# Kernel optimization log

Measured on AMD Instinct MI355X. Metric: run time of the kernel, lower is better.

The kernel has to match this reference:

```python
import jax, jax.numpy as jnp
import numpy as np

BN_EPS = 1e-5
NN_EPS = 1e-8
K = 3


def conv_bn_relu(x, W, b, gamma, beta, mean, var):
    # x: [B, Cin, N]; W: [Cout, Cin] (1x1 conv); BN in inference mode w/ running stats
    y = jnp.einsum('bcn,oc->bon', x, W) + b[None, :, None]
    y = (y - mean[None, :, None]) * (gamma / jnp.sqrt(var + BN_EPS))[None, :, None] + beta[None, :, None]
    return jax.nn.relu(y)


def three_interpolation(p1, p2, f2):
    # p1: [B, N1, 3] unknown xyz; p2: [B, N2, 3] known xyz; f2: [B, C, N2]
    # squared pairwise distances via the expansion trick (avoids [B,N1,N2,3])
    d2 = (jnp.sum(p1 * p1, -1)[:, :, None]
          + jnp.sum(p2 * p2, -1)[:, None, :]
          - 2.0 * jnp.einsum('bnd,bmd->bnm', p1, p2))  # [B, N1, N2]
    neg_d2, idx = jax.lax.top_k(-d2, K)                 # 3 nearest
    dist = -neg_d2                                      # squared dists, [B, N1, 3]
    recip = 1.0 / (dist + NN_EPS)
    weight = recip / jnp.sum(recip, axis=-1, keepdims=True)  # [B, N1, 3]
    f2t = jnp.transpose(f2, (0, 2, 1))                  # [B, N2, C]
    gathered = jax.vmap(lambda f, i: f[i])(f2t, idx)    # [B, N1, 3, C]
    return jnp.einsum('bnkc,bnk->bcn', gathered, weight)  # [B, C, N1]


def setup_inputs() -> dict:
    key = jax.random.key(0)
    ks = jax.random.split(key, 16)
    B, N1, N2 = 8, 16384, 4096
    mlp = [256, 128, 128]
    inp = {
        'p1': jax.random.normal(ks[0], (B, N1, 3), jnp.float32),
        'p2': jax.random.normal(ks[1], (B, N2, 3), jnp.float32),
        'f2': jax.random.normal(ks[2], (B, mlp[0], N2), jnp.float32),
    }
    kidx = 3
    for li in range(len(mlp) - 1):
        cin, cout = mlp[li], mlp[li + 1]
        inp[f'W{li}'] = jax.random.normal(ks[kidx], (cout, cin), jnp.float32) * (1.0 / np.sqrt(cin)); kidx += 1
        inp[f'b{li}'] = jnp.zeros((cout,), jnp.float32)
        inp[f'gamma{li}'] = jnp.ones((cout,), jnp.float32)
        inp[f'beta{li}'] = jnp.zeros((cout,), jnp.float32)
        inp[f'mean{li}'] = jax.random.normal(ks[kidx], (cout,), jnp.float32) * 0.1; kidx += 1
        inp[f'var{li}'] = jax.random.uniform(ks[kidx], (cout,), jnp.float32, 0.5, 1.5); kidx += 1
    return inp


def reference(p1, p2, f2,
              W0, b0, gamma0, beta0, mean0, var0,
              W1, b1, gamma1, beta1, mean1, var1):
    f = conv_bn_relu(f2, W0, b0, gamma0, beta0, mean0, var0)
    f = conv_bn_relu(f, W1, b1, gamma1, beta1, mean1, var1)
    return three_interpolation(p1, p2, f)
```

## Files before the change

kernel.cpp:

```cpp
#include <hip/hip_runtime.h>

#define B_    8
#define N1_   16384
#define N2_   4096
#define NTOT_ (B_ * N1_)

__device__ __forceinline__ float np_sumsq(float x, float y, float z)
{
#pragma clang fp contract(off)
    return ((x * x + y * y) + z * z);
}

__global__ __launch_bounds__(256) void prep_kernel(
    const float* __restrict__ W0, const float* __restrict__ b0,
    const float* __restrict__ g0, const float* __restrict__ be0,
    const float* __restrict__ m0, const float* __restrict__ v0,
    const float* __restrict__ W1, const float* __restrict__ b1,
    const float* __restrict__ g1, const float* __restrict__ be1,
    const float* __restrict__ m1, const float* __restrict__ v1,
    const float* __restrict__ p2,
    float* __restrict__ W0p, float* __restrict__ b0p,
    float* __restrict__ W1p, float* __restrict__ b1p,
    float4* __restrict__ q4)
{
    const int bx = blockIdx.x;
    const int tid = threadIdx.x;
    if (bx < 128) {
        const int t = bx * 256 + tid;
        const int o = t >> 8;
        const float s = g0[o] / sqrtf(v0[o] + 1e-5f);
        W0p[t] = W0[t] * s;
        if (t < 128) {
            const float ss = g0[t] / sqrtf(v0[t] + 1e-5f);
            b0p[t] = be0[t] + (b0[t] - m0[t]) * ss;
        }
    } else if (bx < 192) {
        const int t = (bx - 128) * 256 + tid;
        const int o = t >> 7;
        const float s = g1[o] / sqrtf(v1[o] + 1e-5f);
        W1p[t] = W1[t] * s;
        if (t < 128) {
            const float ss = g1[t] / sqrtf(v1[t] + 1e-5f);
            b1p[t] = be1[t] + (b1[t] - m1[t]) * ss;
        }
    } else {
        const int t = (bx - 192) * 256 + tid;
        const float x = p2[3 * (size_t)t + 0];
        const float y = p2[3 * (size_t)t + 1];
        const float z = p2[3 * (size_t)t + 2];
        q4[t] = make_float4(x, y, z, np_sumsq(x, y, z));
    }
}

template <int CIN, bool TRANS>
__global__ __launch_bounds__(256) void gemm_relu_kernel(
    const float* __restrict__ X, const float* __restrict__ Wp,
    const float* __restrict__ bp, float* __restrict__ Y)
{
    __shared__ float A_lds[32][136];
    __shared__ float B_lds[32][64];

    const int b  = blockIdx.y;
    const int n0 = blockIdx.x * 64;
    const int tid = threadIdx.x;
    const int ty = tid >> 4;
    const int tx = tid & 15;
    const float* Xb = X + (size_t)b * CIN * N2_;

    float acc[8][4];
#pragma unroll
    for (int i = 0; i < 8; ++i)
#pragma unroll
        for (int j = 0; j < 4; ++j) acc[i][j] = 0.f;

    const int a_kq = (tid & 7) * 4;
    const int a_r0 = tid >> 3;
    const int b_n4 = (tid & 15) * 4;
    const int b_k0 = tid >> 4;

    for (int k0 = 0; k0 < CIN; k0 += 32) {
#pragma unroll
        for (int i = 0; i < 4; ++i) {
            const int row = a_r0 + 32 * i;
            const float4 v = *(const float4*)&Wp[(size_t)row * CIN + k0 + a_kq];
            A_lds[a_kq + 0][row] = v.x;
            A_lds[a_kq + 1][row] = v.y;
            A_lds[a_kq + 2][row] = v.z;
            A_lds[a_kq + 3][row] = v.w;
        }
#pragma unroll
        for (int i = 0; i < 2; ++i) {
            const int krow = b_k0 + 16 * i;
            *(float4*)&B_lds[krow][b_n4] =
                *(const float4*)&Xb[(size_t)(k0 + krow) * N2_ + n0 + b_n4];
        }
        __syncthreads();

#pragma unroll
        for (int kk = 0; kk < 32; ++kk) {
            const float4 a0 = *(const float4*)&A_lds[kk][ty * 4];
            const float4 a1 = *(const float4*)&A_lds[kk][64 + ty * 4];
            const float4 bq = *(const float4*)&B_lds[kk][tx * 4];
            const float av[8] = {a0.x, a0.y, a0.z, a0.w, a1.x, a1.y, a1.z, a1.w};
            const float bv[4] = {bq.x, bq.y, bq.z, bq.w};
#pragma unroll
            for (int i = 0; i < 8; ++i)
#pragma unroll
                for (int j = 0; j < 4; ++j)
                    acc[i][j] = fmaf(av[i], bv[j], acc[i][j]);
        }
        __syncthreads();
    }

    float bias_v[8];
#pragma unroll
    for (int i = 0; i < 8; ++i) {
        const int r = (i < 4) ? (ty * 4 + i) : (64 + ty * 4 + (i - 4));
        bias_v[i] = bp[r];
    }

    if (!TRANS) {
#pragma unroll
        for (int i = 0; i < 8; ++i) {
            const int r = (i < 4) ? (ty * 4 + i) : (64 + ty * 4 + (i - 4));
            float* yrow = Y + ((size_t)b * 128 + r) * N2_ + n0;
            float4 v0;
            v0.x = fmaxf(acc[i][0] + bias_v[i], 0.f);
            v0.y = fmaxf(acc[i][1] + bias_v[i], 0.f);
            v0.z = fmaxf(acc[i][2] + bias_v[i], 0.f);
            v0.w = fmaxf(acc[i][3] + bias_v[i], 0.f);
            *(float4*)(yrow + tx * 4) = v0;
        }
    } else {
        float (*T)[132] = (float(*)[132])&A_lds[0][0];
#pragma unroll
        for (int s = 0; s < 2; ++s) {
            if ((tx >> 3) == s) {
                const int cl0 = (tx & 7) * 4;
#pragma unroll
                for (int i = 0; i < 8; ++i) {
                    const int r = (i < 4) ? (ty * 4 + i) : (64 + ty * 4 + (i - 4));
#pragma unroll
                    for (int j = 0; j < 4; ++j)
                        T[cl0 + j][r] = fmaxf(acc[i][j] + bias_v[i], 0.f);
                }
            }
            __syncthreads();
#pragma unroll
            for (int p = 0; p < 4; ++p) {
                const int row = (tid >> 5) + 8 * p;
                const float4 v = *(const float4*)&T[row][(tid & 31) * 4];
                float* orow = Y + ((size_t)b * N2_ + n0 + 32 * s + row) * 128;
                *(float4*)&orow[(tid & 31) * 4] = v;
            }
            __syncthreads();
        }
    }
}

__global__ __launch_bounds__(256, 8) void knn_phase1(
    const float* __restrict__ p1, const float4* __restrict__ q4,
    float* __restrict__ part_d, int* __restrict__ part_i)
{
    __shared__ float4 qs[1024];
    const int tid = threadIdx.x;
    const int chunk = blockIdx.x & 3;
    const int g = (blockIdx.x >> 2) * 256 + tid;
    const int b = g >> 14;

    const float px = p1[3 * (size_t)g + 0];
    const float py = p1[3 * (size_t)g + 1];
    const float pz = p1[3 * (size_t)g + 2];
    const float s1 = np_sumsq(px, py, pz);

    const float4* qb = q4 + (size_t)b * N2_ + chunk * 1024;
#pragma unroll
    for (int i = 0; i < 4; ++i) qs[tid + i * 256] = qb[tid + i * 256];
    __syncthreads();

    float d0 = 1e30f, d1 = 1e30f, d2v = 1e30f;
    int i0 = 0, i1 = 0, i2 = 0;
    const int jbase = chunk * 1024;

    for (int j = 0; j < 1024; j += 4) {
#pragma unroll
        for (int u = 0; u < 4; ++u) {
            const float4 q = qs[j + u];
            const float dot = __fmaf_rn(px, q.x, __fmaf_rn(py, q.y, __fmul_rn(pz, q.z)));
            const float ss  = s1 + q.w;
            const float t   = __fmaf_rn(-2.0f, dot, ss);
            if (t < d2v) {
                const int jj = jbase + j + u;
                const bool c1 = t < d1, c0 = t < d0;
                d2v = c1 ? d1 : t;                 i2 = c1 ? i1 : jj;
                const float nd1 = c1 ? (c0 ? d0 : t) : d1;
                const int   ni1 = c1 ? (c0 ? i0 : jj) : i1;
                d1 = nd1;                          i1 = ni1;
                d0 = c0 ? t : d0;                  i0 = c0 ? jj : i0;
            }
        }
    }

    part_d[(0 * 4 + chunk) * NTOT_ + g] = d0;
    part_d[(1 * 4 + chunk) * NTOT_ + g] = d1;
    part_d[(2 * 4 + chunk) * NTOT_ + g] = d2v;
    part_i[(0 * 4 + chunk) * NTOT_ + g] = i0;
    part_i[(1 * 4 + chunk) * NTOT_ + g] = i1;
    part_i[(2 * 4 + chunk) * NTOT_ + g] = i2;
}

__global__ __launch_bounds__(256) void gather_kernel(
    const float* __restrict__ f_t, const float* __restrict__ part_d,
    const int* __restrict__ part_i, float* __restrict__ out)
{
    const int tid = threadIdx.x;
    const int lane = tid & 63, cg = tid >> 6;
    const int vb = (blockIdx.x & 7) * 256 + (blockIdx.x >> 3);
    const int g = vb * 64 + lane;
    const int b = g >> 14, n = g & 16383;

    float d0 = 1e30f, d1 = 1e30f, d2v = 1e30f;
    int i0 = 0, i1 = 0, i2 = 0;
#pragma unroll
    for (int c = 0; c < 4; ++c) {
#pragma unroll
        for (int k = 0; k < 3; ++k) {
            const float t = part_d[(k * 4 + c) * NTOT_ + g];
            const int  jj = part_i[(k * 4 + c) * NTOT_ + g];
            if (t < d2v) {
                const bool c1 = t < d1, c0 = t < d0;
                d2v = c1 ? d1 : t;                 i2 = c1 ? i1 : jj;
                const float nd1 = c1 ? (c0 ? d0 : t) : d1;
                const int   ni1 = c1 ? (c0 ? i0 : jj) : i1;
                d1 = nd1;                          i1 = ni1;
                d0 = c0 ? t : d0;                  i0 = c0 ? jj : i0;
            }
        }
    }

    float w0, w1, w2;
    {
#pragma clang fp contract(off)
        const float r0 = 1.0f / (d0 + 1e-8f);
        const float r1 = 1.0f / (d1 + 1e-8f);
        const float r2 = 1.0f / (d2v + 1e-8f);
        const float rs = (r0 + r1) + r2;
        w0 = r0 / rs;
        w1 = r1 / rs;
        w2 = r2 / rs;
    }

    const float* base = f_t + (size_t)b * N2_ * 128 + cg * 32;
    const float4* r0v = (const float4*)(base + (size_t)i0 * 128);
    const float4* r1v = (const float4*)(base + (size_t)i1 * 128);
    const float4* r2v = (const float4*)(base + (size_t)i2 * 128);

    float acc[32];
#pragma unroll
    for (int q = 0; q < 8; ++q) {
        const float4 a = r0v[q], bb = r1v[q], c = r2v[q];
        acc[4 * q + 0] = fmaf(w0, a.x, fmaf(w1, bb.x, w2 * c.x));
        acc[4 * q + 1] = fmaf(w0, a.y, fmaf(w1, bb.y, w2 * c.y));
        acc[4 * q + 2] = fmaf(w0, a.z, fmaf(w1, bb.z, w2 * c.z));
        acc[4 * q + 3] = fmaf(w0, a.w, fmaf(w1, bb.w, w2 * c.w));
    }

    float* ob = out + ((size_t)b * 128 + cg * 32) * N1_ + n;
#pragma unroll
    for (int c = 0; c < 32; ++c)
        __builtin_nontemporal_store(acc[c], ob + (size_t)c * N1_);
}

extern "C" void kernel_launch(void* const* d_in, const int* in_sizes, int n_in,
                              void* d_out, int out_size, void* d_ws, size_t ws_size,
                              hipStream_t stream)
{
    const float* p1  = (const float*)d_in[0];
    const float* p2  = (const float*)d_in[1];
    const float* f2  = (const float*)d_in[2];
    const float* W0  = (const float*)d_in[3];
    const float* b0  = (const float*)d_in[4];
    const float* g0  = (const float*)d_in[5];
    const float* be0 = (const float*)d_in[6];
    const float* m0  = (const float*)d_in[7];
    const float* v0  = (const float*)d_in[8];
    const float* W1  = (const float*)d_in[9];
    const float* b1  = (const float*)d_in[10];
    const float* g1  = (const float*)d_in[11];
    const float* be1 = (const float*)d_in[12];
    const float* m1  = (const float*)d_in[13];
    const float* v1  = (const float*)d_in[14];

    char* ws = (char*)d_ws;
    float4* q4  = (float4*)(ws);
    float*  W0p = (float*)(ws + (512 << 10));
    float*  b0p = (float*)(ws + (640 << 10));
    float*  W1p = (float*)(ws + (644 << 10));
    float*  b1p = (float*)(ws + (708 << 10));
    float*  h   = (float*)(ws + ((size_t)1 << 20));
    float*  f_t = (float*)(ws + ((size_t)17 << 20));
    float*  pd  = (float*)(ws + ((size_t)1 << 20));
    int*    pi  = (int*)  (ws + ((size_t)9 << 20));

    prep_kernel<<<320, 256, 0, stream>>>(W0, b0, g0, be0, m0, v0,
                                         W1, b1, g1, be1, m1, v1,
                                         p2, W0p, b0p, W1p, b1p, q4);

    gemm_relu_kernel<256, false><<<dim3(64, 8), 256, 0, stream>>>(f2, W0p, b0p, h);
    gemm_relu_kernel<128, true ><<<dim3(64, 8), 256, 0, stream>>>(h, W1p, b1p, f_t);

    knn_phase1<<<(NTOT_ / 256) * 4, 256, 0, stream>>>(p1, q4, pd, pi);
    gather_kernel<<<NTOT_ / 64, 256, 0, stream>>>(f_t, pd, pi, (float*)d_out);
}
```

Before: 354.4 us.

## Co-schedule KNN distance chunks with the two 1x1-conv GEMMs in mixed kernels

Merges each GEMM+ReLU stage with half of the KNN phase-1 work into a single launch. Blocks below 512 run the GEMM and the remaining blocks scan two of the four point chunks, sharing a union of LDS buffers. The aim is to fill the GPU, since each GEMM alone launches only 512 blocks, and to drop one kernel launch. The partial-result buffers move to new workspace offsets so they no longer alias h. A __launch_bounds__ occupancy hint of 6 is added, which may constrain registers for the KNN path.

```diff
diff --git a/kernel.cpp b/kernel.cpp
--- a/kernel.cpp
+++ b/kernel.cpp
@@ -52,161 +52,166 @@
     }
 }
 
-template <int CIN, bool TRANS>
-__global__ __launch_bounds__(256) void gemm_relu_kernel(
+template <int PHASE>
+__global__ __launch_bounds__(256, 6) void mix_kernel(
     const float* __restrict__ X, const float* __restrict__ Wp,
-    const float* __restrict__ bp, float* __restrict__ Y)
-{
-    __shared__ float A_lds[32][136];
-    __shared__ float B_lds[32][64];
-
-    const int b  = blockIdx.y;
-    const int n0 = blockIdx.x * 64;
+    const float* __restrict__ bp, float* __restrict__ Y,
+    const float* __restrict__ p1, const float4* __restrict__ q4,
+    float* __restrict__ part_d, int* __restrict__ part_i)
+{
+    constexpr int  CIN   = (PHASE == 1) ? 256 : 128;
+    constexpr bool TRANS = (PHASE == 2);
+
+    __shared__ union LdsU {
+        struct { float A[32][136]; float B[32][64]; } g;
+        float4 qs[1024];
+    } lds;
+
     const int tid = threadIdx.x;
-    const int ty = tid >> 4;
-    const int tx = tid & 15;
-    const float* Xb = X + (size_t)b * CIN * N2_;
-
-    float acc[8][4];
-#pragma unroll
-    for (int i = 0; i < 8; ++i)
-#pragma unroll
-        for (int j = 0; j < 4; ++j) acc[i][j] = 0.f;
-
-    const int a_kq = (tid & 7) * 4;
-    const int a_r0 = tid >> 3;
-    const int b_n4 = (tid & 15) * 4;
-    const int b_k0 = tid >> 4;
-
-    for (int k0 = 0; k0 < CIN; k0 += 32) {
-#pragma unroll
-        for (int i = 0; i < 4; ++i) {
-            const int row = a_r0 + 32 * i;
-            const float4 v = *(const float4*)&Wp[(size_t)row * CIN + k0 + a_kq];
-            A_lds[a_kq + 0][row] = v.x;
-            A_lds[a_kq + 1][row] = v.y;
-            A_lds[a_kq + 2][row] = v.z;
-            A_lds[a_kq + 3][row] = v.w;
-        }
-#pragma unroll
-        for (int i = 0; i < 2; ++i) {
-            const int krow = b_k0 + 16 * i;
-            *(float4*)&B_lds[krow][b_n4] =
-                *(const float4*)&Xb[(size_t)(k0 + krow) * N2_ + n0 + b_n4];
-        }
-        __syncthreads();
-
-#pragma unroll
-        for (int kk = 0; kk < 32; ++kk) {
-            const float4 a0 = *(const float4*)&A_lds[kk][ty * 4];
-            const float4 a1 = *(const float4*)&A_lds[kk][64 + ty * 4];
-            const float4 bq = *(const float4*)&B_lds[kk][tx * 4];
-            const float av[8] = {a0.x, a0.y, a0.z, a0.w, a1.x, a1.y, a1.z, a1.w};
-            const float bv[4] = {bq.x, bq.y, bq.z, bq.w};
-#pragma unroll
-            for (int i = 0; i < 8; ++i)
-#pragma unroll
-                for (int j = 0; j < 4; ++j)
-                    acc[i][j] = fmaf(av[i], bv[j], acc[i][j]);
-        }
-        __syncthreads();
-    }
-
-    float bias_v[8];
-#pragma unroll
-    for (int i = 0; i < 8; ++i) {
-        const int r = (i < 4) ? (ty * 4 + i) : (64 + ty * 4 + (i - 4));
-        bias_v[i] = bp[r];
-    }
-
-    if (!TRANS) {
+    const int bx  = blockIdx.x;
+
+    if (bx < 512) {
+        const int b  = bx >> 6;
+        const int n0 = (bx & 63) * 64;
+        const int ty = tid >> 4;
+        const int tx = tid & 15;
+        const float* Xb = X + (size_t)b * CIN * N2_;
+
+        float acc[8][4];
+#pragma unroll
+        for (int i = 0; i < 8; ++i)
+#pragma unroll
+            for (int j = 0; j < 4; ++j) acc[i][j] = 0.f;
+
+        const int a_kq = (tid & 7) * 4;
+        const int a_r0 = tid >> 3;
+        const int b_n4 = (tid & 15) * 4;
+        const int b_k0 = tid >> 4;
+
+        for (int k0 = 0; k0 < CIN; k0 += 32) {
+#pragma unroll
+            for (int i = 0; i < 4; ++i) {
+                const int row = a_r0 + 32 * i;
+                const float4 v = *(const float4*)&Wp[(size_t)row * CIN + k0 + a_kq];
+                lds.g.A[a_kq + 0][row] = v.x;
+                lds.g.A[a_kq + 1][row] = v.y;
+                lds.g.A[a_kq + 2][row] = v.z;
+                lds.g.A[a_kq + 3][row] = v.w;
+            }
+#pragma unroll
+            for (int i = 0; i < 2; ++i) {
+                const int krow = b_k0 + 16 * i;
+                *(float4*)&lds.g.B[krow][b_n4] =
+                    *(const float4*)&Xb[(size_t)(k0 + krow) * N2_ + n0 + b_n4];
+            }
+            __syncthreads();
+
+#pragma unroll
+            for (int kk = 0; kk < 32; ++kk) {
+                const float4 a0 = *(const float4*)&lds.g.A[kk][ty * 4];
+                const float4 a1 = *(const float4*)&lds.g.A[kk][64 + ty * 4];
+                const float4 bq = *(const float4*)&lds.g.B[kk][tx * 4];
+                const float av[8] = {a0.x, a0.y, a0.z, a0.w, a1.x, a1.y, a1.z, a1.w};
+                const float bv[4] = {bq.x, bq.y, bq.z, bq.w};
+#pragma unroll
+                for (int i = 0; i < 8; ++i)
+#pragma unroll
+                    for (int j = 0; j < 4; ++j)
+                        acc[i][j] = fmaf(av[i], bv[j], acc[i][j]);
+            }
+            __syncthreads();
+        }
+
+        float bias_v[8];
 #pragma unroll
         for (int i = 0; i < 8; ++i) {
             const int r = (i < 4) ? (ty * 4 + i) : (64 + ty * 4 + (i - 4));
-            float* yrow = Y + ((size_t)b * 128 + r) * N2_ + n0;
-            float4 v0;
-            v0.x = fmaxf(acc[i][0] + bias_v[i], 0.f);
-            v0.y = fmaxf(acc[i][1] + bias_v[i], 0.f);
-            v0.z = fmaxf(acc[i][2] + bias_v[i], 0.f);
-            v0.w = fmaxf(acc[i][3] + bias_v[i], 0.f);
-            *(float4*)(yrow + tx * 4) = v0;
+            bias_v[i] = bp[r];
+        }
+
+        if (!TRANS) {
+#pragma unroll
+            for (int i = 0; i < 8; ++i) {
+                const int r = (i < 4) ? (ty * 4 + i) : (64 + ty * 4 + (i - 4));
+                float* yrow = Y + ((size_t)b * 128 + r) * N2_ + n0;
+                float4 v0;
+                v0.x = fmaxf(acc[i][0] + bias_v[i], 0.f);
+                v0.y = fmaxf(acc[i][1] + bias_v[i], 0.f);
+                v0.z = fmaxf(acc[i][2] + bias_v[i], 0.f);
+                v0.w = fmaxf(acc[i][3] + bias_v[i], 0.f);
+                *(float4*)(yrow + tx * 4) = v0;
+            }
+        } else {
+            float (*T)[132] = (float(*)[132])&lds.g.A[0][0];
+#pragma unroll
+            for (int s = 0; s < 2; ++s) {
+                if ((tx >> 3) == s) {
+                    const int cl0 = (tx & 7) * 4;
+#pragma unroll
+                    for (int i = 0; i < 8; ++i) {
+                        const int r = (i < 4) ? (ty * 4 + i) : (64 + ty * 4 + (i - 4));
+#pragma unroll
+                        for (int j = 0; j < 4; ++j)
+                            T[cl0 + j][r] = fmaxf(acc[i][j] + bias_v[i], 0.f);
+                    }
+                }
+                __syncthreads();
+#pragma unroll
+                for (int p = 0; p < 4; ++p) {
+                    const int row = (tid >> 5) + 8 * p;
+                    const float4 v = *(const float4*)&T[row][(tid & 31) * 4];
+                    float* orow = Y + ((size_t)b * N2_ + n0 + 32 * s + row) * 128;
+                    *(float4*)&orow[(tid & 31) * 4] = v;
+                }
+                __syncthreads();
+            }
         }
     } else {
-        float (*T)[132] = (float(*)[132])&A_lds[0][0];
-#pragma unroll
-        for (int s = 0; s < 2; ++s) {
-            if ((tx >> 3) == s) {
-                const int cl0 = (tx & 7) * 4;
-#pragma unroll
-                for (int i = 0; i < 8; ++i) {
-                    const int r = (i < 4) ? (ty * 4 + i) : (64 + ty * 4 + (i - 4));
-#pragma unroll
-                    for (int j = 0; j < 4; ++j)
-                        T[cl0 + j][r] = fmaxf(acc[i][j] + bias_v[i], 0.f);
+        const int bxk = bx - 512;
+        const int chunk = (bxk & 1) + ((PHASE - 1) << 1);
+        const int g = (bxk >> 1) * 256 + tid;
+        const int b = g >> 14;
+
+        const float px = p1[3 * (size_t)g + 0];
+        const float py = p1[3 * (size_t)g + 1];
+        const float pz = p1[3 * (size_t)g + 2];
+        const float s1 = np_sumsq(px, py, pz);
+
+        const float4* qb = q4 + (size_t)b * N2_ + chunk * 1024;
+#pragma unroll
+        for (int i = 0; i < 4; ++i) lds.qs[tid + i * 256] = qb[tid + i * 256];
+        __syncthreads();
+
+        float d0 = 1e30f, d1 = 1e30f, d2v = 1e30f;
+        int i0 = 0, i1 = 0, i2 = 0;
+        const int jbase = chunk * 1024;
+
+        for (int j = 0; j < 1024; j += 4) {
+#pragma unroll
+            for (int u = 0; u < 4; ++u) {
+                const float4 q = lds.qs[j + u];
+                const float dot = __fmaf_rn(px, q.x, __fmaf_rn(py, q.y, __fmul_rn(pz, q.z)));
+                const float ss  = s1 + q.w;
+                const float t   = __fmaf_rn(-2.0f, dot, ss);
+                if (t < d2v) {
+                    const int jj = jbase + j + u;
+                    const bool c1 = t < d1, c0 = t < d0;
+                    d2v = c1 ? d1 : t;                 i2 = c1 ? i1 : jj;
+                    const float nd1 = c1 ? (c0 ? d0 : t) : d1;
+                    const int   ni1 = c1 ? (c0 ? i0 : jj) : i1;
+                    d1 = nd1;                          i1 = ni1;
+                    d0 = c0 ? t : d0;                  i0 = c0 ? jj : i0;
                 }
             }
-            __syncthreads();
-#pragma unroll
-            for (int p = 0; p < 4; ++p) {
-                const int row = (tid >> 5) + 8 * p;
-                const float4 v = *(const float4*)&T[row][(tid & 31) * 4];
-                float* orow = Y + ((size_t)b * N2_ + n0 + 32 * s + row) * 128;
-                *(float4*)&orow[(tid & 31) * 4] = v;
-            }
-            __syncthreads();
-        }
-    }
-}
-
-__global__ __launch_bounds__(256, 8) void knn_phase1(
-    const float* __restrict__ p1, const float4* __restrict__ q4,
-    float* __restrict__ part_d, int* __restrict__ part_i)
-{
-    __shared__ float4 qs[1024];
-    const int tid = threadIdx.x;
-    const int chunk = blockIdx.x & 3;
-    const int g = (blockIdx.x >> 2) * 256 + tid;
-    const int b = g >> 14;
-
-    const float px = p1[3 * (size_t)g + 0];
-    const float py = p1[3 * (size_t)g + 1];
-    const float pz = p1[3 * (size_t)g + 2];
-    const float s1 = np_sumsq(px, py, pz);
-
-    const float4* qb = q4 + (size_t)b * N2_ + chunk * 1024;
-#pragma unroll
-    for (int i = 0; i < 4; ++i) qs[tid + i * 256] = qb[tid + i * 256];
-    __syncthreads();
-
-    float d0 = 1e30f, d1 = 1e30f, d2v = 1e30f;
-    int i0 = 0, i1 = 0, i2 = 0;
-    const int jbase = chunk * 1024;
-
-    for (int j = 0; j < 1024; j += 4) {
-#pragma unroll
-        for (int u = 0; u < 4; ++u) {
-            const float4 q = qs[j + u];
-            const float dot = __fmaf_rn(px, q.x, __fmaf_rn(py, q.y, __fmul_rn(pz, q.z)));
-            const float ss  = s1 + q.w;
-            const float t   = __fmaf_rn(-2.0f, dot, ss);
-            if (t < d2v) {
-                const int jj = jbase + j + u;
-                const bool c1 = t < d1, c0 = t < d0;
-                d2v = c1 ? d1 : t;                 i2 = c1 ? i1 : jj;
-                const float nd1 = c1 ? (c0 ? d0 : t) : d1;
-                const int   ni1 = c1 ? (c0 ? i0 : jj) : i1;
-                d1 = nd1;                          i1 = ni1;
-                d0 = c0 ? t : d0;                  i0 = c0 ? jj : i0;
-            }
-        }
-    }
-
-    part_d[(0 * 4 + chunk) * NTOT_ + g] = d0;
-    part_d[(1 * 4 + chunk) * NTOT_ + g] = d1;
-    part_d[(2 * 4 + chunk) * NTOT_ + g] = d2v;
-    part_i[(0 * 4 + chunk) * NTOT_ + g] = i0;
-    part_i[(1 * 4 + chunk) * NTOT_ + g] = i1;
-    part_i[(2 * 4 + chunk) * NTOT_ + g] = i2;
+        }
+
+        part_d[(0 * 4 + chunk) * NTOT_ + g] = d0;
+        part_d[(1 * 4 + chunk) * NTOT_ + g] = d1;
+        part_d[(2 * 4 + chunk) * NTOT_ + g] = d2v;
+        part_i[(0 * 4 + chunk) * NTOT_ + g] = i0;
+        part_i[(1 * 4 + chunk) * NTOT_ + g] = i1;
+        part_i[(2 * 4 + chunk) * NTOT_ + g] = i2;
+    }
 }
 
 __global__ __launch_bounds__(256) void gather_kernel(
@@ -299,16 +304,17 @@
     float*  b1p = (float*)(ws + (708 << 10));
     float*  h   = (float*)(ws + ((size_t)1 << 20));
     float*  f_t = (float*)(ws + ((size_t)17 << 20));
-    float*  pd  = (float*)(ws + ((size_t)1 << 20));
-    int*    pi  = (int*)  (ws + ((size_t)9 << 20));
+    float*  pd  = (float*)(ws + ((size_t)33 << 20));
+    int*    pi  = (int*)  (ws + ((size_t)40 << 20));
 
     prep_kernel<<<320, 256, 0, stream>>>(W0, b0, g0, be0, m0, v0,
                                          W1, b1, g1, be1, m1, v1,
                                          p2, W0p, b0p, W1p, b1p, q4);
 
-    gemm_relu_kernel<256, false><<<dim3(64, 8), 256, 0, stream>>>(f2, W0p, b0p, h);
-    gemm_relu_kernel<128, true ><<<dim3(64, 8), 256, 0, stream>>>(h, W1p, b1p, f_t);
-
-    knn_phase1<<<(NTOT_ / 256) * 4, 256, 0, stream>>>(p1, q4, pd, pi);
+    mix_kernel<1><<<1536, 256, 0, stream>>>(f2, W0p, b0p, h,
+                                            p1, q4, pd, pi);
+    mix_kernel<2><<<1536, 256, 0, stream>>>(h, W1p, b1p, f_t,
+                                            p1, q4, pd, pi);
+
     gather_kernel<<<NTOT_ / 64, 256, 0, stream>>>(f_t, pd, pi, (float*)d_out);
 }
```

Result: slower. 388.9 us (+9.7%).

## Gather neighbor feature rows cooperatively per wave and transpose through LDS

Applied to the files above, without the earlier changes.

Each wave previously had every lane fetch its own point's 32-channel slice from three random neighbor rows, so the gathers were uncoalesced. Now the wave broadcasts one point's indices and weights with shuffles, and all 64 lanes read that point's full 128-channel rows contiguously as float2. The blended values go into a padded shared-memory tile and are written out transposed with coalesced stores. This adds 33 KB of LDS per block and a barrier, and all four waves redundantly compute the same top-3 merge.

```diff
diff --git a/kernel.cpp b/kernel.cpp
--- a/kernel.cpp
+++ b/kernel.cpp
@@ -213,11 +213,13 @@
     const float* __restrict__ f_t, const float* __restrict__ part_d,
     const int* __restrict__ part_i, float* __restrict__ out)
 {
+    __shared__ float T[64][129];
     const int tid = threadIdx.x;
-    const int lane = tid & 63, cg = tid >> 6;
+    const int lane = tid & 63, wv = tid >> 6;
     const int vb = (blockIdx.x & 7) * 256 + (blockIdx.x >> 3);
-    const int g = vb * 64 + lane;
-    const int b = g >> 14, n = g & 16383;
+    const int gbase = vb * 64;
+    const int g = gbase + lane;
+    const int b = g >> 14, n0 = gbase & 16383;
 
     float d0 = 1e30f, d1 = 1e30f, d2v = 1e30f;
     int i0 = 0, i1 = 0, i2 = 0;
@@ -250,25 +252,30 @@
         w2 = r2 / rs;
     }
 
-    const float* base = f_t + (size_t)b * N2_ * 128 + cg * 32;
-    const float4* r0v = (const float4*)(base + (size_t)i0 * 128);
-    const float4* r1v = (const float4*)(base + (size_t)i1 * 128);
-    const float4* r2v = (const float4*)(base + (size_t)i2 * 128);
-
-    float acc[32];
-#pragma unroll
-    for (int q = 0; q < 8; ++q) {
-        const float4 a = r0v[q], bb = r1v[q], c = r2v[q];
-        acc[4 * q + 0] = fmaf(w0, a.x, fmaf(w1, bb.x, w2 * c.x));
-        acc[4 * q + 1] = fmaf(w0, a.y, fmaf(w1, bb.y, w2 * c.y));
-        acc[4 * q + 2] = fmaf(w0, a.z, fmaf(w1, bb.z, w2 * c.z));
-        acc[4 * q + 3] = fmaf(w0, a.w, fmaf(w1, bb.w, w2 * c.w));
-    }
-
-    float* ob = out + ((size_t)b * 128 + cg * 32) * N1_ + n;
-#pragma unroll
-    for (int c = 0; c < 32; ++c)
-        __builtin_nontemporal_store(acc[c], ob + (size_t)c * N1_);
+    const float* fb = f_t + (size_t)b * N2_ * 128;
+#pragma unroll
+    for (int j = 0; j < 16; ++j) {
+        const int q = wv * 16 + j;
+        const int   qi0 = __shfl(i0, q);
+        const int   qi1 = __shfl(i1, q);
+        const int   qi2 = __shfl(i2, q);
+        const float qw0 = __shfl(w0, q);
+        const float qw1 = __shfl(w1, q);
+        const float qw2 = __shfl(w2, q);
+        const float2 a  = *(const float2*)(fb + (size_t)qi0 * 128 + 2 * lane);
+        const float2 bb = *(const float2*)(fb + (size_t)qi1 * 128 + 2 * lane);
+        const float2 c  = *(const float2*)(fb + (size_t)qi2 * 128 + 2 * lane);
+        T[q][2 * lane + 0] = fmaf(qw0, a.x, fmaf(qw1, bb.x, qw2 * c.x));
+        T[q][2 * lane + 1] = fmaf(qw0, a.y, fmaf(qw1, bb.y, qw2 * c.y));
+    }
+    __syncthreads();
+
+    float* ob = out + ((size_t)b * 128) * N1_ + n0 + lane;
+#pragma unroll
+    for (int ci = 0; ci < 32; ++ci) {
+        const int cch = wv * 32 + ci;
+        __builtin_nontemporal_store(T[lane][cch], ob + (size_t)cch * N1_);
+    }
 }
 
 extern "C" void kernel_launch(void* const* d_in, const int* in_sizes, int n_in,
```

After: 333.3 us. -5.9%, faster.
